# Kernel optimization log

Hardware: AMD Instinct MI355X
Metric: run time of the kernel (lower is better)

The kernel has to match this reference:

```python
import jax, jax.numpy as jnp
import numpy as np

STD = 0.01

def setup_inputs() -> dict:
    key = jax.random.key(0)
    k1, k2, k3 = jax.random.split(key, 3)
    B, T, D = 16, 4096, 512
    x = jax.random.normal(k1, (B, T, D), dtype=jnp.float32)
    att_W = jax.random.normal(k2, (D, D), dtype=jnp.float32) * STD
    att_v = jax.random.normal(k3, (D,), dtype=jnp.float32) * STD
    return {"x": x, "att_W": att_W, "att_v": att_v}

def reference(x, att_W, att_v):
    # additive attention scores: tanh(x @ W) @ v -> [B, T]
    y = jnp.tanh(jnp.einsum('btd,de->bte', x, att_W))
    scores = jnp.einsum('btd,d->bt', y, att_v)
    weights = jax.nn.softmax(scores, axis=-1)          # softmax over sequence
    out = jnp.einsum('bt,btd->bd', weights, x)         # weighted sum pooling
    return out.astype(jnp.float32)
```

## Files before the change

### kernel.cpp

```cpp
#include <hip/hip_runtime.h>
#include <hip/hip_bf16.h>
#include <math.h>

#define BB 16
#define TT 4096
#define DD 512
#define MM (BB*TT)

typedef __bf16 bf16x8 __attribute__((ext_vector_type(8)));
typedef float  f32x4  __attribute__((ext_vector_type(4)));

__device__ inline unsigned short f2bf(float f) {
    unsigned u = __builtin_bit_cast(unsigned, f) + 0x8000u;
    return (unsigned short)(u >> 16);
}

__device__ inline unsigned pack_bf16x2(float lo, float hi) {
    unsigned u0 = __builtin_bit_cast(unsigned, lo) + 0x8000u;
    unsigned u1 = __builtin_bit_cast(unsigned, hi) + 0x8000u;
    return __builtin_amdgcn_perm(u1, u0, 0x07060302);
}

__device__ inline float tanh_fast(float y) {
    float e = __expf(2.0f * y);
    return 1.0f - 2.0f * __builtin_amdgcn_rcpf(e + 1.0f);
}

__global__ void wb_kernel(const float* __restrict__ W, unsigned short* __restrict__ Wb) {
    int u = blockIdx.x * 256 + threadIdx.x;
    int lane = u & 63;
    int ni   = (u >> 6) & 1;
    int s    = (u >> 7) & 15;
    int p    = (u >> 11) & 3;
    int wid  = u >> 13;
    int n  = ((p * 4 + wid) * 2 + ni) * 16 + (lane & 15);
    int k0 = s * 32 + (lane >> 4) * 8;
    unsigned short o[8];
    #pragma unroll
    for (int j = 0; j < 8; j++) o[j] = f2bf(W[(size_t)(k0 + j) * DD + n]);
    *(uint4*)(Wb + (size_t)u * 8) = *(uint4*)o;
}

__global__ __launch_bounds__(256, 2) void scores_kernel(
        const float* __restrict__ x, const unsigned short* __restrict__ Wb,
        const float* __restrict__ v, float* __restrict__ scores) {
    __shared__ unsigned short As[64 * DD];
    __shared__ float sbuf[4][64];

    const int tid  = threadIdx.x;
    const int m0   = blockIdx.x * 64;
    const int wid  = tid >> 6;
    const int lane = tid & 63;
    const int l15  = lane & 15;
    const int q    = lane >> 4;
    const int r3   = l15 & 7;

    const unsigned short* bqp = Wb + ((size_t)wid << 16) + lane * 8;

    bf16x8 b[4][2];
    #pragma unroll
    for (int g = 0; g < 3; g++) {
        b[g][0] = *(const bf16x8*)(bqp);
        b[g][1] = *(const bf16x8*)(bqp + 512);
        bqp += 1024;
    }

    #pragma unroll 4
    for (int i = 0; i < 16; i++) {
        int u = i * 256 + tid;
        int r = u >> 6;
        int c = u & 63;
        const float* gp = x + (size_t)(m0 + r) * DD + c * 8;
        float4 f0 = *(const float4*)(gp);
        float4 f1 = *(const float4*)(gp + 4);
        uint4 o;
        o.x = pack_bf16x2(f0.x, f0.y);
        o.y = pack_bf16x2(f0.z, f0.w);
        o.z = pack_bf16x2(f1.x, f1.y);
        o.w = pack_bf16x2(f1.z, f1.w);
        *(uint4*)(&As[r * DD + (c ^ (r & 7)) * 8]) = o;
    }
    __syncthreads();

    float vpart[4][4];
    #pragma unroll
    for (int mi = 0; mi < 4; mi++)
        #pragma unroll
        for (int rr = 0; rr < 4; rr++)
            vpart[mi][rr] = 0.f;

#define A_FRAG(mi, s) (*(const bf16x8*)(&As[((mi)*16 + l15) * DD + ((((s)*4 + q) ^ r3) * 8)]))

    bf16x8 a[2][4];
    #pragma unroll
    for (int mi = 0; mi < 4; mi++) a[0][mi] = A_FRAG(mi, 0);

    #pragma unroll
    for (int p = 0; p < 4; p++) {
        f32x4 acc[4][2];
        #pragma unroll
        for (int mi = 0; mi < 4; mi++)
            #pragma unroll
            for (int ni = 0; ni < 2; ni++)
                acc[mi][ni] = (f32x4){0.f, 0.f, 0.f, 0.f};

        #pragma unroll
        for (int s = 0; s < 16; s++) {
            const int g   = p * 16 + s;
            const int cur = g & 1;
            if (g < 63) {
                const int ns = (s + 1) & 15;
                #pragma unroll
                for (int mi = 0; mi < 4; mi++) a[cur ^ 1][mi] = A_FRAG(mi, ns);
            }
            if (g < 61) {
                b[(g + 3) & 3][0] = *(const bf16x8*)(bqp);
                b[(g + 3) & 3][1] = *(const bf16x8*)(bqp + 512);
                bqp += 1024;
            }
            #pragma unroll
            for (int mi = 0; mi < 4; mi++)
                #pragma unroll
                for (int ni = 0; ni < 2; ni++)
                    acc[mi][ni] = __builtin_amdgcn_mfma_f32_16x16x32_bf16(
                        a[cur][mi], b[g & 3][ni], acc[mi][ni], 0, 0, 0);
        }

        float vv[2];
        vv[0] = v[(p * 4 + wid) * 32 + l15];
        vv[1] = v[(p * 4 + wid) * 32 + 16 + l15];
        #pragma unroll
        for (int mi = 0; mi < 4; mi++)
            #pragma unroll
            for (int ni = 0; ni < 2; ni++)
                #pragma unroll
                for (int rr = 0; rr < 4; rr++)
                    vpart[mi][rr] += tanh_fast(acc[mi][ni][rr]) * vv[ni];
    }
#undef A_FRAG

    #pragma unroll
    for (int mi = 0; mi < 4; mi++)
        #pragma unroll
        for (int rr = 0; rr < 4; rr++) {
            float sum = vpart[mi][rr];
            sum += __shfl_xor(sum, 1);
            sum += __shfl_xor(sum, 2);
            sum += __shfl_xor(sum, 4);
            sum += __shfl_xor(sum, 8);
            if (l15 == 0)
                sbuf[wid][mi * 16 + q * 4 + rr] = sum;
        }
    __syncthreads();
    if (tid < 64)
        scores[m0 + tid] = sbuf[0][tid] + sbuf[1][tid] + sbuf[2][tid] + sbuf[3][tid];
}

__global__ void softmax_kernel(const float* __restrict__ scores, float* __restrict__ weights) {
    const int b = blockIdx.x;
    const int tid = threadIdx.x;
    __shared__ float wred[4];

    float s[16];
    float mx = -1e30f;
    #pragma unroll
    for (int i = 0; i < 16; i++) {
        float sv = scores[b * TT + i * 256 + tid];
        s[i] = sv;
        mx = fmaxf(mx, sv);
    }
    #pragma unroll
    for (int off = 32; off; off >>= 1) mx = fmaxf(mx, __shfl_xor(mx, off));
    if ((tid & 63) == 0) wred[tid >> 6] = mx;
    __syncthreads();
    mx = fmaxf(fmaxf(wred[0], wred[1]), fmaxf(wred[2], wred[3]));
    __syncthreads();

    float sum = 0.f;
    #pragma unroll
    for (int i = 0; i < 16; i++) { s[i] = __expf(s[i] - mx); sum += s[i]; }
    #pragma unroll
    for (int off = 32; off; off >>= 1) sum += __shfl_xor(sum, off);
    if ((tid & 63) == 0) wred[tid >> 6] = sum;
    __syncthreads();
    sum = wred[0] + wred[1] + wred[2] + wred[3];

    const float inv = 1.0f / sum;
    #pragma unroll
    for (int i = 0; i < 16; i++)
        weights[b * TT + i * 256 + tid] = s[i] * inv;
}

#define PTCH 64
__global__ __launch_bounds__(256) void pool_kernel(
        const float* __restrict__ x, const float* __restrict__ weights,
        float* __restrict__ out) {
    __shared__ float wsm[PTCH];
    __shared__ f32x4 psum[128];
    const int b   = blockIdx.y;
    const int t0  = blockIdx.x * PTCH;
    const int tid = threadIdx.x;
    if (tid < PTCH) wsm[tid] = weights[b * TT + t0 + tid];
    __syncthreads();

    const int dq = tid & 127;
    const int ts = tid >> 7;
    f32x4 acc = (f32x4){0.f, 0.f, 0.f, 0.f};
    const float* xp = x + ((size_t)b * TT + t0 + ts) * DD + dq * 4;
    #pragma unroll 8
    for (int t = ts; t < PTCH; t += 2) {
        f32x4 xv = *(const f32x4*)xp;
        acc += wsm[t] * xv;
        xp += 2 * DD;
    }
    if (ts == 1) psum[dq] = acc;
    __syncthreads();
    if (ts == 0) {
        acc += psum[dq];
        float* op = out + b * DD + dq * 4;
        atomicAdd(op + 0, acc[0]);
        atomicAdd(op + 1, acc[1]);
        atomicAdd(op + 2, acc[2]);
        atomicAdd(op + 3, acc[3]);
    }
}

extern "C" void kernel_launch(void* const* d_in, const int* in_sizes, int n_in,
                              void* d_out, int out_size, void* d_ws, size_t ws_size,
                              hipStream_t stream) {
    (void)in_sizes; (void)n_in; (void)out_size; (void)ws_size;
    const float* x = (const float*)d_in[0];
    const float* W = (const float*)d_in[1];
    const float* v = (const float*)d_in[2];
    float* out = (float*)d_out;

    unsigned short* Wb = (unsigned short*)d_ws;
    float* scores      = (float*)((char*)d_ws + 512 * 1024);
    float* weights     = (float*)((char*)d_ws + 512 * 1024 + 256 * 1024);

    hipMemsetAsync(d_out, 0, BB * DD * sizeof(float), stream);

    wb_kernel<<<128, 256, 0, stream>>>(W, Wb);

    scores_kernel<<<MM / 64, 256, 0, stream>>>(x, Wb, v, scores);

    softmax_kernel<<<BB, 256, 0, stream>>>(scores, weights);

    pool_kernel<<<dim3(TT / PTCH, BB), 256, 0, stream>>>(x, weights, out);
}
```

Baseline: 290.1 us.

## Fuse softmax and pooling into scores kernel using LDS-resident bf16 x tile

Scores, per-block softmax partials (max, sum-exp) and exp-weighted pooling are computed in one kernel, reusing the bf16 x tile already in LDS. A small combine kernel merges per-block partials with online-softmax rescaling. This removes the second full read of x from global memory, the scores/weights round trips, the memset and the atomics. Pooling now uses bf16-rounded x, lowering accuracy, and the wave split changes to 2x2, doubling B fragment loads per wave.

```diff
diff --git a/kernel.cpp b/kernel.cpp
--- a/kernel.cpp
+++ b/kernel.cpp
@@ -29,11 +29,12 @@
 __global__ void wb_kernel(const float* __restrict__ W, unsigned short* __restrict__ Wb) {
     int u = blockIdx.x * 256 + threadIdx.x;
     int lane = u & 63;
-    int ni   = (u >> 6) & 1;
-    int s    = (u >> 7) & 15;
-    int p    = (u >> 11) & 3;
-    int wid  = u >> 13;
-    int n  = ((p * 4 + wid) * 2 + ni) * 16 + (lane & 15);
+    int fid  = u >> 6;
+    int ni = fid & 1;
+    int s  = (fid >> 1) & 15;
+    int p  = (fid >> 5) & 7;
+    int h  = fid >> 8;
+    int n  = h * 256 + p * 32 + ni * 16 + (lane & 15);
     int k0 = s * 32 + (lane >> 4) * 8;
     unsigned short o[8];
     #pragma unroll
@@ -41,11 +42,15 @@
     *(uint4*)(Wb + (size_t)u * 8) = *(uint4*)o;
 }
 
-__global__ __launch_bounds__(256, 2) void scores_kernel(
+__global__ __launch_bounds__(256, 2) void scorepool_kernel(
         const float* __restrict__ x, const unsigned short* __restrict__ Wb,
-        const float* __restrict__ v, float* __restrict__ scores) {
+        const float* __restrict__ v,
+        float* __restrict__ num_ws, float* __restrict__ mz_ws) {
     __shared__ unsigned short As[64 * DD];
-    __shared__ float sbuf[4][64];
+    __shared__ float sbuf[2][64];
+    __shared__ float ew[64];
+    __shared__ float mzsh[2];
+    __shared__ float psum[4][DD];
 
     const int tid  = threadIdx.x;
     const int m0   = blockIdx.x * 64;
@@ -54,16 +59,8 @@
     const int l15  = lane & 15;
     const int q    = lane >> 4;
     const int r3   = l15 & 7;
-
-    const unsigned short* bqp = Wb + ((size_t)wid << 16) + lane * 8;
-
-    bf16x8 b[4][2];
-    #pragma unroll
-    for (int g = 0; g < 3; g++) {
-        b[g][0] = *(const bf16x8*)(bqp);
-        b[g][1] = *(const bf16x8*)(bqp + 512);
-        bqp += 1024;
-    }
+    const int wr   = (wid & 1) * 32;
+    const int wh   = wid >> 1;
 
     #pragma unroll 4
     for (int i = 0; i < 16; i++) {
@@ -80,67 +77,70 @@
         o.w = pack_bf16x2(f1.z, f1.w);
         *(uint4*)(&As[r * DD + (c ^ (r & 7)) * 8]) = o;
     }
-    __syncthreads();
-
-    float vpart[4][4];
-    #pragma unroll
-    for (int mi = 0; mi < 4; mi++)
+
+    const unsigned short* bqp = Wb + (size_t)wh * 131072 + lane * 8;
+    bf16x8 b[4][2];
+    #pragma unroll
+    for (int g = 0; g < 3; g++) {
+        b[g][0] = *(const bf16x8*)(bqp);
+        b[g][1] = *(const bf16x8*)(bqp + 512);
+        bqp += 1024;
+    }
+
+    __syncthreads();
+
+    float vpart[2][4];
+    #pragma unroll
+    for (int mi = 0; mi < 2; mi++)
         #pragma unroll
         for (int rr = 0; rr < 4; rr++)
             vpart[mi][rr] = 0.f;
 
-#define A_FRAG(mi, s) (*(const bf16x8*)(&As[((mi)*16 + l15) * DD + ((((s)*4 + q) ^ r3) * 8)]))
-
-    bf16x8 a[2][4];
-    #pragma unroll
-    for (int mi = 0; mi < 4; mi++) a[0][mi] = A_FRAG(mi, 0);
-
-    #pragma unroll
-    for (int p = 0; p < 4; p++) {
-        f32x4 acc[4][2];
-        #pragma unroll
-        for (int mi = 0; mi < 4; mi++)
+#define A_FRAG(mi, s) (*(const bf16x8*)(&As[(wr + (mi)*16 + l15) * DD + ((((s)*4 + q) ^ r3) * 8)]))
+
+    bf16x8 a[2][2];
+    a[0][0] = A_FRAG(0, 0);
+    a[0][1] = A_FRAG(1, 0);
+
+    #pragma unroll 1
+    for (int p = 0; p < 8; p++) {
+        f32x4 acc[2][2];
+        #pragma unroll
+        for (int mi = 0; mi < 2; mi++)
             #pragma unroll
             for (int ni = 0; ni < 2; ni++)
                 acc[mi][ni] = (f32x4){0.f, 0.f, 0.f, 0.f};
 
         #pragma unroll
         for (int s = 0; s < 16; s++) {
-            const int g   = p * 16 + s;
-            const int cur = g & 1;
-            if (g < 63) {
-                const int ns = (s + 1) & 15;
-                #pragma unroll
-                for (int mi = 0; mi < 4; mi++) a[cur ^ 1][mi] = A_FRAG(mi, ns);
-            }
-            if (g < 61) {
-                b[(g + 3) & 3][0] = *(const bf16x8*)(bqp);
-                b[(g + 3) & 3][1] = *(const bf16x8*)(bqp + 512);
-                bqp += 1024;
-            }
+            const int cur = s & 1;
+            const int ns  = (s + 1) & 15;
+            a[cur ^ 1][0] = A_FRAG(0, ns);
+            a[cur ^ 1][1] = A_FRAG(1, ns);
+            b[(s + 3) & 3][0] = *(const bf16x8*)(bqp);
+            b[(s + 3) & 3][1] = *(const bf16x8*)(bqp + 512);
+            bqp += 1024;
             #pragma unroll
-            for (int mi = 0; mi < 4; mi++)
+            for (int mi = 0; mi < 2; mi++)
                 #pragma unroll
                 for (int ni = 0; ni < 2; ni++)
                     acc[mi][ni] = __builtin_amdgcn_mfma_f32_16x16x32_bf16(
-                        a[cur][mi], b[g & 3][ni], acc[mi][ni], 0, 0, 0);
+                        a[cur][mi], b[s & 3][ni], acc[mi][ni], 0, 0, 0);
         }
 
-        float vv[2];
-        vv[0] = v[(p * 4 + wid) * 32 + l15];
-        vv[1] = v[(p * 4 + wid) * 32 + 16 + l15];
-        #pragma unroll
-        for (int mi = 0; mi < 4; mi++)
+        float vv0 = v[wh * 256 + p * 32 + l15];
+        float vv1 = v[wh * 256 + p * 32 + 16 + l15];
+        #pragma unroll
+        for (int mi = 0; mi < 2; mi++)
             #pragma unroll
-            for (int ni = 0; ni < 2; ni++)
-                #pragma unroll
-                for (int rr = 0; rr < 4; rr++)
-                    vpart[mi][rr] += tanh_fast(acc[mi][ni][rr]) * vv[ni];
+            for (int rr = 0; rr < 4; rr++)
+                vpart[mi][rr] += tanh_fast(acc[mi][0][rr]) * vv0
+                               + tanh_fast(acc[mi][1][rr]) * vv1;
     }
 #undef A_FRAG
 
     #pragma unroll
-    for (int mi = 0; mi < 4; mi++)
+    for (int mi = 0; mi < 2; mi++)
         #pragma unroll
         for (int rr = 0; rr < 4; rr++) {
             float sum = vpart[mi][rr];
@@ -149,80 +149,95 @@
             sum += __shfl_xor(sum, 4);
             sum += __shfl_xor(sum, 8);
             if (l15 == 0)
-                sbuf[wid][mi * 16 + q * 4 + rr] = sum;
+                sbuf[wh][wr + mi * 16 + q * 4 + rr] = sum;
         }
     __syncthreads();
-    if (tid < 64)
-        scores[m0 + tid] = sbuf[0][tid] + sbuf[1][tid] + sbuf[2][tid] + sbuf[3][tid];
-}
-
-__global__ void softmax_kernel(const float* __restrict__ scores, float* __restrict__ weights) {
-    const int b = blockIdx.x;
+
+    if (tid < 64) {
+        float s = sbuf[0][tid] + sbuf[1][tid];
+        float m = s;
+        #pragma unroll
+        for (int off = 32; off; off >>= 1) m = fmaxf(m, __shfl_xor(m, off));
+        float e = __expf(s - m);
+        float z = e;
+        #pragma unroll
+        for (int off = 32; off; off >>= 1) z += __shfl_xor(z, off);
+        ew[tid] = e;
+        if (tid == 0) { mzsh[0] = m; mzsh[1] = z; }
+    }
+    __syncthreads();
+
+    const int cx = tid & 63;
+    const int rg = tid >> 6;
+    float nacc[8];
+    #pragma unroll
+    for (int j = 0; j < 8; j++) nacc[j] = 0.f;
+    #pragma unroll 4
+    for (int i = 0; i < 16; i++) {
+        int r = rg * 16 + i;
+        uint4 u = *(const uint4*)(&As[r * DD + ((cx ^ (r & 7)) * 8)]);
+        float e = ew[r];
+        nacc[0] += e * __builtin_bit_cast(float, u.x << 16);
+        nacc[1] += e * __builtin_bit_cast(float, u.x & 0xFFFF0000u);
+        nacc[2] += e * __builtin_bit_cast(float, u.y << 16);
+        nacc[3] += e * __builtin_bit_cast(float, u.y & 0xFFFF0000u);
+        nacc[4] += e * __builtin_bit_cast(float, u.z << 16);
+        nacc[5] += e * __builtin_bit_cast(float, u.z & 0xFFFF0000u);
+        nacc[6] += e * __builtin_bit_cast(float, u.w << 16);
+        nacc[7] += e * __builtin_bit_cast(float, u.w & 0xFFFF0000u);
+    }
+    *(float4*)(&psum[rg][cx * 8])     = *(float4*)(&nacc[0]);
+    *(float4*)(&psum[rg][cx * 8 + 4]) = *(float4*)(&nacc[4]);
+    __syncthreads();
+
+    if (tid < 128) {
+        int c = tid * 4;
+        f32x4 f = *(const f32x4*)(&psum[0][c]);
+        f += *(const f32x4*)(&psum[1][c]);
+        f += *(const f32x4*)(&psum[2][c]);
+        f += *(const f32x4*)(&psum[3][c]);
+        *(f32x4*)(num_ws + (size_t)blockIdx.x * DD + c) = f;
+    }
+    if (tid == 0) {
+        mz_ws[2 * blockIdx.x]     = mzsh[0];
+        mz_ws[2 * blockIdx.x + 1] = mzsh[1];
+    }
+}
+
+__global__ void combine_kernel(const float* __restrict__ num_ws,
+                               const float* __restrict__ mz_ws,
+                               float* __restrict__ out) {
+    __shared__ float fs[64];
+    __shared__ float sinv_sh;
+    const int b   = blockIdx.x;
     const int tid = threadIdx.x;
-    __shared__ float wred[4];
-
-    float s[16];
-    float mx = -1e30f;
-    #pragma unroll
-    for (int i = 0; i < 16; i++) {
-        float sv = scores[b * TT + i * 256 + tid];
-        s[i] = sv;
-        mx = fmaxf(mx, sv);
-    }
-    #pragma unroll
-    for (int off = 32; off; off >>= 1) mx = fmaxf(mx, __shfl_xor(mx, off));
-    if ((tid & 63) == 0) wred[tid >> 6] = mx;
-    __syncthreads();
-    mx = fmaxf(fmaxf(wred[0], wred[1]), fmaxf(wred[2], wred[3]));
-    __syncthreads();
-
-    float sum = 0.f;
-    #pragma unroll
-    for (int i = 0; i < 16; i++) { s[i] = __expf(s[i] - mx); sum += s[i]; }
-    #pragma unroll
-    for (int off = 32; off; off >>= 1) sum += __shfl_xor(sum, off);
-    if ((tid & 63) == 0) wred[tid >> 6] = sum;
-    __syncthreads();
-    sum = wred[0] + wred[1] + wred[2] + wred[3];
-
-    const float inv = 1.0f / sum;
-    #pragma unroll
-    for (int i = 0; i < 16; i++)
-        weights[b * TT + i * 256 + tid] = s[i] * inv;
-}
-
-#define PTCH 64
-__global__ __launch_bounds__(256) void pool_kernel(
-        const float* __restrict__ x, const float* __restrict__ weights,
-        float* __restrict__ out) {
-    __shared__ float wsm[PTCH];
-    __shared__ f32x4 psum[128];
-    const int b   = blockIdx.y;
-    const int t0  = blockIdx.x * PTCH;
-    const int tid = threadIdx.x;
-    if (tid < PTCH) wsm[tid] = weights[b * TT + t0 + tid];
-    __syncthreads();
-
-    const int dq = tid & 127;
-    const int ts = tid >> 7;
-    f32x4 acc = (f32x4){0.f, 0.f, 0.f, 0.f};
-    const float* xp = x + ((size_t)b * TT + t0 + ts) * DD + dq * 4;
-    #pragma unroll 8
-    for (int t = ts; t < PTCH; t += 2) {
-        f32x4 xv = *(const f32x4*)xp;
-        acc += wsm[t] * xv;
-        xp += 2 * DD;
-    }
-    if (ts == 1) psum[dq] = acc;
-    __syncthreads();
-    if (ts == 0) {
-        acc += psum[dq];
-        float* op = out + b * DD + dq * 4;
-        atomicAdd(op + 0, acc[0]);
-        atomicAdd(op + 1, acc[1]);
-        atomicAdd(op + 2, acc[2]);
-        atomicAdd(op + 3, acc[3]);
-    }
+
+    if (tid < 64) {
+        float m = mz_ws[(b * 64 + tid) * 2];
+        float z = mz_ws[(b * 64 + tid) * 2 + 1];
+        float M = m;
+        #pragma unroll
+        for (int off = 32; off; off >>= 1) M = fmaxf(M, __shfl_xor(M, off));
+        float f  = __expf(m - M);
+        float fz = f * z;
+        #pragma unroll
+        for (int off = 32; off; off >>= 1) fz += __shfl_xor(fz, off);
+        fs[tid] = f;
+        if (tid == 0) sinv_sh = 1.0f / fz;
+    }
+    __syncthreads();
+
+    float a0 = 0.f, a1 = 0.f;
+    #pragma unroll 4
+    for (int c = 0; c < 64; c++) {
+        float f = fs[c];
+        const float* np = num_ws + (size_t)(b * 64 + c) * DD;
+        a0 += f * np[tid];
+        a1 += f * np[tid + 256];
+    }
+    const float sinv = sinv_sh;
+    out[b * DD + tid]       = a0 * sinv;
+    out[b * DD + tid + 256] = a1 * sinv;
 }
 
 extern "C" void kernel_launch(void* const* d_in, const int* in_sizes, int n_in,
@@ -235,16 +250,12 @@
     float* out = (float*)d_out;
 
     unsigned short* Wb = (unsigned short*)d_ws;
-    float* scores      = (float*)((char*)d_ws + 512 * 1024);
-    float* weights     = (float*)((char*)d_ws + 512 * 1024 + 256 * 1024);
-
-    hipMemsetAsync(d_out, 0, BB * DD * sizeof(float), stream);
+    float* num_ws      = (float*)((char*)d_ws + 512 * 1024 + 8 * 1024);
+    float* mz_ws       = (float*)((char*)d_ws + 512 * 1024 + 8 * 1024 + 2 * 1024 * 1024);
 
     wb_kernel<<<128, 256, 0, stream>>>(W, Wb);
 
-    scores_kernel<<<MM / 64, 256, 0, stream>>>(x, Wb, v, scores);
-
-    softmax_kernel<<<BB, 256, 0, stream>>>(scores, weights);
-
-    pool_kernel<<<dim3(TT / PTCH, BB), 256, 0, stream>>>(x, weights, out);
-}
+    scorepool_kernel<<<MM / 64, 256, 0, stream>>>(x, Wb, v, num_ws, mz_ws);
+
+    combine_kernel<<<BB, 256, 0, stream>>>(num_ws, mz_ws, out);
+}
```

Measured after the change: 254.7 us. -12.2%, faster.
